# Kernel optimization log

Hardware: AMD Instinct MI355X
Metric: run time of the kernel (lower is better)

Reference implementation:

```python
import jax, jax.numpy as jnp
import numpy as np

B, T, C = 2, 2048, 1024
H = 16
HS = C // H  # head_size = 64


def setup_inputs() -> dict:
    key = jax.random.key(0)
    k1, k2, k3 = jax.random.split(key, 3)
    x = jax.random.normal(k1, (B, T, C), dtype=jnp.float32)
    # nn.Linear(n_embd, 3*n_embd): weight [3C, C], bias [3C]
    W = jax.random.normal(k2, (3 * C, C), dtype=jnp.float32) * (C ** -0.5)
    b = jax.random.normal(k3, (3 * C,), dtype=jnp.float32) * 0.02
    return {"x": x, "W": W, "b": b}


def reference(x, W, b):
    Bs, Ts, Cs = x.shape
    # fused QKV projection: [B,T,3C]
    qkv = x @ W.T + b
    qkv = qkv.reshape(Bs, Ts, 3, H, HS)
    q, k, v = jnp.moveaxis(qkv, 2, 0)          # each [B,T,H,HS]
    q = q.transpose(0, 2, 1, 3)                 # [B,H,T,HS]
    k = k.transpose(0, 2, 1, 3)
    v = v.transpose(0, 2, 1, 3)
    scale = HS ** -0.5
    wei = jnp.einsum('bhqd,bhkd->bhqk', q, k) * scale  # [B,H,T,T]
    causal = jnp.tril(jnp.ones((Ts, Ts), dtype=bool))
    wei = jnp.where(causal, wei, -jnp.inf)
    wei = jax.nn.softmax(wei, axis=-1)
    out = jnp.einsum('bhqk,bhkd->bhqd', wei, v)        # [B,H,T,HS]
    return out.transpose(0, 2, 1, 3).reshape(Bs, Ts, Cs)
```

## Files before the change

kernel.cpp:

```cpp
#include <hip/hip_runtime.h>
#include <hip/hip_bf16.h>

typedef __attribute__((ext_vector_type(8))) short bf16x8;
typedef __attribute__((ext_vector_type(4))) float f32x4;

#define BATCH 2
#define T_SEQ 2048
#define C_EMB 1024
#define NH 16
#define HS 64

__device__ __forceinline__ void gld_lds16(const __hip_bfloat16* g, __hip_bfloat16* l) {
    __builtin_amdgcn_global_load_lds((const __attribute__((address_space(1))) uint32_t*)g,
                                     (__attribute__((address_space(3))) uint32_t*)l, 16, 0, 0);
}

__global__ void cvt_f32_bf16(const float4* __restrict__ s0, ushort4* __restrict__ d0, int n40,
                             const float4* __restrict__ s1, ushort4* __restrict__ d1, int n41) {
    int i = blockIdx.x * blockDim.x + threadIdx.x;
    const float4* s; ushort4* d; int j;
    if (i < n40)            { s = s0; d = d0; j = i; }
    else if (i < n40 + n41) { s = s1; d = d1; j = i - n40; }
    else return;
    float4 v = s[j];
    ushort4 o;
    __hip_bfloat16 h;
    h = __float2bfloat16(v.x); o.x = *(ushort*)&h;
    h = __float2bfloat16(v.y); o.y = *(ushort*)&h;
    h = __float2bfloat16(v.z); o.z = *(ushort*)&h;
    h = __float2bfloat16(v.w); o.w = *(ushort*)&h;
    d[j] = o;
}

#define NT_K 16

__launch_bounds__(512, 2)
__global__ void qkv_gemm(const __hip_bfloat16* __restrict__ xb,
                         const __hip_bfloat16* __restrict__ wb,
                         const float* __restrict__ bias,
                         __hip_bfloat16* __restrict__ qo,
                         __hip_bfloat16* __restrict__ ko,
                         __hip_bfloat16* __restrict__ vto)
{
    __shared__ __align__(16) char smem[131072];
    __hip_bfloat16* ASB = (__hip_bfloat16*)smem;
    __hip_bfloat16* BSB = (__hip_bfloat16*)(smem + 65536);
    const int K = C_EMB;
    const int nTn = (3 * C_EMB) / 256;
    int bid = blockIdx.x;
    int wgid = (bid & 7) * 24 + (bid >> 3);
    int bm = wgid / nTn, bn = wgid % nTn;
    int m0 = bm * 256, n0 = bn * 256;
    int tid  = threadIdx.x;
    int lane = tid & 63, w = tid >> 6;
    int wr = w >> 2, wc = w & 3;
    int c = lane & 15, g = lane >> 4;
    int sr = lane >> 2;
    int sj = (lane & 3) ^ ((sr >> 1) & 3);
    int rchnk = (g ^ ((c >> 1) & 3)) << 4;

#define STAGE_A(kt, kh, buf) \
    { _Pragma("unroll") for (int i_ = 0; i_ < 2; ++i_) { \
        int r0_ = w * 32 + i_ * 16; \
        gld_lds16(&xb[(size_t)(m0 + r0_ + sr) * K + (kt) * 64 + (kh) * 32 + sj * 8], \
                  &ASB[((buf) * 2 + (kh)) * 8192 + r0_ * 32]); } }
#define STAGE_B(kt, kh, buf) \
    { _Pragma("unroll") for (int i_ = 0; i_ < 2; ++i_) { \
        int r0_ = w * 32 + i_ * 16; \
        gld_lds16(&wb[(size_t)(n0 + r0_ + sr) * K + (kt) * 64 + (kh) * 32 + sj * 8], \
                  &BSB[((buf) * 2 + (kh)) * 8192 + r0_ * 32]); } }

    f32x4 acc[8][4];
#pragma unroll
    for (int mi = 0; mi < 8; ++mi)
#pragma unroll
        for (int ni = 0; ni < 4; ++ni)
            acc[mi][ni] = (f32x4){0.f, 0.f, 0.f, 0.f};

    STAGE_A(0, 0, 0); STAGE_B(0, 0, 0);
    STAGE_A(0, 1, 0); STAGE_B(0, 1, 0);
    STAGE_A(1, 0, 1); STAGE_B(1, 0, 1);
    asm volatile("s_waitcnt vmcnt(4)" ::: "memory");
    __builtin_amdgcn_s_barrier();

    for (int t = 0; t < NT_K; ++t) {
        int buf = t & 1;
#pragma unroll
        for (int ks = 0; ks < 2; ++ks) {
            const __hip_bfloat16* AL = &ASB[(buf * 2 + ks) * 8192];
            const __hip_bfloat16* BL = &BSB[(buf * 2 + ks) * 8192];
            bf16x8 af[8], bfr[4];
#pragma unroll
            for (int mi = 0; mi < 8; ++mi)
                af[mi] = *(const bf16x8*)((const char*)AL + (wr * 128 + mi * 16 + c) * 64 + rchnk);
#pragma unroll
            for (int ni = 0; ni < 4; ++ni)
                bfr[ni] = *(const bf16x8*)((const char*)BL + (wc * 64 + ni * 16 + c) * 64 + rchnk);
            if (ks == 0) {
                if (t + 1 < NT_K) { STAGE_A(t + 1, 1, buf ^ 1); STAGE_B(t + 1, 1, buf ^ 1); }
            } else {
                if (t + 2 < NT_K) { STAGE_A(t + 2, 0, buf); STAGE_B(t + 2, 0, buf); }
            }
            __builtin_amdgcn_s_barrier();
            asm volatile("s_waitcnt lgkmcnt(0)" ::: "memory");
            __builtin_amdgcn_s_setprio(1);
#pragma unroll
            for (int mi = 0; mi < 8; ++mi)
#pragma unroll
                for (int ni = 0; ni < 4; ++ni)
                    acc[mi][ni] = __builtin_amdgcn_mfma_f32_16x16x32_bf16(af[mi], bfr[ni], acc[mi][ni], 0, 0, 0);
            __builtin_amdgcn_s_setprio(0);
            if (ks == 1) {
                if (t + 2 < NT_K) asm volatile("s_waitcnt vmcnt(4)" ::: "memory");
                else              asm volatile("s_waitcnt vmcnt(0)" ::: "memory");
            }
            __builtin_amdgcn_s_barrier();
        }
    }
#undef STAGE_A
#undef STAGE_B

    const float QSCALE = 0.125f * 1.44269504088896340736f;
    if (bn < 8) {
        const bool isQ = (bn < 4);
        __hip_bfloat16* dst = isQ ? qo : ko;
        float scale = isQ ? QSCALE : 1.0f;
        int h = (bn * 4 + wc) & (NH - 1);
        int b = m0 >> 11;
        size_t bhb = (size_t)(b * NH + h) * T_SEQ;
#pragma unroll
        for (int ni = 0; ni < 4; ++ni) {
            int d = ni * 16 + c;
            float bv = bias[n0 + wc * 64 + d];
#pragma unroll
            for (int mi = 0; mi < 8; ++mi) {
#pragma unroll
                for (int r = 0; r < 4; ++r) {
                    int tt = (m0 & (T_SEQ - 1)) + wr * 128 + mi * 16 + g * 4 + r;
                    float v = (acc[mi][ni][r] + bv) * scale;
                    dst[(bhb + tt) * HS + d] = __float2bfloat16(v);
                }
            }
        }
    } else {
        __syncthreads();
        char* tb = smem + w * 16384;
        int h = (bn - 8) * 4 + wc;
#pragma unroll
        for (int ni = 0; ni < 4; ++ni) {
            int d = ni * 16 + c;
            float bv = bias[n0 + wc * 64 + d];
#pragma unroll
            for (int mi = 0; mi < 8; ++mi) {
#pragma unroll
                for (int r = 0; r < 4; ++r) {
                    int m = mi * 16 + g * 4 + r;
                    __hip_bfloat16 hv = __float2bfloat16(acc[mi][ni][r] + bv);
                    *(ushort*)(tb + d * 256 + (((m >> 3) ^ c) << 4) + (m & 7) * 2) = *(ushort*)&hv;
                }
            }
        }
        int b = m0 >> 11;
        int t0 = (m0 & (T_SEQ - 1)) + wr * 128;
        size_t bh = (size_t)(b * NH + h);
        int c2 = lane & 15, g2 = lane >> 4;
#pragma unroll
        for (int it = 0; it < 16; ++it) {
            int d = it * 4 + g2;
            bf16x8 vv = *(bf16x8*)(tb + d * 256 + ((c2 ^ (d & 15)) << 4));
            *(bf16x8*)(&vto[(bh * HS + d) * T_SEQ + t0 + c2 * 8]) = vv;
        }
    }
}

#define PLDT 72

__launch_bounds__(256, 2)
__global__ void attn_fwd(const __hip_bfloat16* __restrict__ qb,
                         const __hip_bfloat16* __restrict__ kb,
                         const __hip_bfloat16* __restrict__ vtb,
                         float* __restrict__ out)
{
    __shared__ __align__(16) __hip_bfloat16 k_lds[3][64 * 64];
    __shared__ __align__(16) __hip_bfloat16 v_lds[3][64 * 64];
    __shared__ __align__(16) __hip_bfloat16 p_lds_all[4][16 * PLDT];

    int bh = blockIdx.x & 31;
    int pp = blockIdx.x >> 5;
    int w  = threadIdx.x >> 6;
    int lane = threadIdx.x & 63;
    int c = lane & 15, g = lane >> 4;
    __hip_bfloat16* p_lds = p_lds_all[w];

    const __hip_bfloat16* Qp = qb  + (size_t)bh * T_SEQ * HS;
    const __hip_bfloat16* Kp = kb  + (size_t)bh * T_SEQ * HS;
    const __hip_bfloat16* Vp = vtb + (size_t)bh * HS * T_SEQ;
    int b = bh >> 4, h = bh & (NH - 1);

    int srow = lane >> 3;
    int scol = ((lane & 7) ^ srow) << 3;
    int swz  = (c & 7) << 4;
    int krow0 = w * 16 + srow;
    int krow1 = w * 16 + 8 + srow;

    for (int phase = 0; phase < 2; ++phase) {
        int qt = phase ? pp : 31 - pp;
        int qw = qt * 64 + w * 16;
        int ntile = qt + 1;

        bf16x8 qf[2];
        qf[0] = *(const bf16x8*)(&Qp[(size_t)(qw + c) * HS + g * 8]);
        qf[1] = *(const bf16x8*)(&Qp[(size_t)(qw + c) * HS + 32 + g * 8]);

        f32x4 oacc[4];
#pragma unroll
        for (int i = 0; i < 4; ++i) oacc[i] = (f32x4){0.f, 0.f, 0.f, 0.f};
        float lrow = 0.f;

        gld_lds16(&Kp[(size_t)krow0 * HS + scol],  &k_lds[0][(w * 16) * 64]);
        gld_lds16(&Kp[(size_t)krow1 * HS + scol],  &k_lds[0][(w * 16 + 8) * 64]);
        gld_lds16(&Vp[(size_t)krow0 * T_SEQ + scol], &v_lds[0][(w * 16) * 64]);
        gld_lds16(&Vp[(size_t)krow1 * T_SEQ + scol], &v_lds[0][(w * 16 + 8) * 64]);

        int cur = 0;
        for (int tix = 0; tix < ntile; ++tix) {
            int nb = cur + 1; if (nb == 3) nb = 0;
            if (tix + 1 < ntile) {
                int k0n = (tix + 1) * 64;
                gld_lds16(&Kp[(size_t)(k0n + krow0) * HS + scol],  &k_lds[nb][(w * 16) * 64]);
                gld_lds16(&Kp[(size_t)(k0n + krow1) * HS + scol],  &k_lds[nb][(w * 16 + 8) * 64]);
                gld_lds16(&Vp[(size_t)krow0 * T_SEQ + k0n + scol], &v_lds[nb][(w * 16) * 64]);
                gld_lds16(&Vp[(size_t)krow1 * T_SEQ + k0n + scol], &v_lds[nb][(w * 16 + 8) * 64]);
                asm volatile("s_waitcnt vmcnt(4)" ::: "memory");
            } else {
                asm volatile("s_waitcnt vmcnt(0)" ::: "memory");
            }
            __builtin_amdgcn_s_barrier();

            bool diag = (tix == ntile - 1);
            const __hip_bfloat16* KL = k_lds[cur];
            const __hip_bfloat16* VL = v_lds[cur];

            f32x4 sacc[4];
#pragma unroll
            for (int i = 0; i < 4; ++i) sacc[i] = (f32x4){0.f, 0.f, 0.f, 0.f};
            __builtin_amdgcn_s_setprio(1);
#pragma unroll
            for (int ks = 0; ks < 2; ++ks)
#pragma unroll
                for (int kc = 0; kc < 4; ++kc)
                    if (!diag || kc <= w) {
                        int rr = kc * 16 + c;
                        int colB = (ks * 64 + g * 16) ^ swz;
                        bf16x8 kf = *(const bf16x8*)(&KL[rr * 64 + (colB >> 1)]);
                        sacc[kc] = __builtin_amdgcn_mfma_f32_16x16x32_bf16(kf, qf[ks], sacc[kc], 0, 0, 0);
                    }
            __builtin_amdgcn_s_setprio(0);

#pragma unroll
            for (int kc = 0; kc < 4; ++kc) {
                float p0, p1, p2, p3;
                if (!diag) {
                    p0 = __builtin_amdgcn_exp2f(sacc[kc][0]);
                    p1 = __builtin_amdgcn_exp2f(sacc[kc][1]);
                    p2 = __builtin_amdgcn_exp2f(sacc[kc][2]);
                    p3 = __builtin_amdgcn_exp2f(sacc[kc][3]);
                } else {
                    int kbase = kc * 16 + g * 4;
                    int lim = w * 16 + c;
                    p0 = (kc <= w && kbase + 0 <= lim) ? __builtin_amdgcn_exp2f(sacc[kc][0]) : 0.f;
                    p1 = (kc <= w && kbase + 1 <= lim) ? __builtin_amdgcn_exp2f(sacc[kc][1]) : 0.f;
                    p2 = (kc <= w && kbase + 2 <= lim) ? __builtin_amdgcn_exp2f(sacc[kc][2]) : 0.f;
                    p3 = (kc <= w && kbase + 3 <= lim) ? __builtin_amdgcn_exp2f(sacc[kc][3]) : 0.f;
                }
                lrow += (p0 + p1) + (p2 + p3);
                unsigned lo = ((__builtin_bit_cast(unsigned, p0) + 0x8000u) >> 16) |
                              ((__builtin_bit_cast(unsigned, p1) + 0x8000u) & 0xffff0000u);
                unsigned hi = ((__builtin_bit_cast(unsigned, p2) + 0x8000u) >> 16) |
                              ((__builtin_bit_cast(unsigned, p3) + 0x8000u) & 0xffff0000u);
                *(uint2*)(&p_lds[c * PLDT + kc * 16 + g * 4]) = make_uint2(lo, hi);
            }

            int ksm = diag ? ((w >= 2) ? 2 : 1) : 2;
            __builtin_amdgcn_s_setprio(1);
#pragma unroll
            for (int ks = 0; ks < 2; ++ks) {
                if (ks >= ksm) break;
                bf16x8 pf = *(bf16x8*)(&p_lds[c * PLDT + ks * 32 + g * 8]);
#pragma unroll
                for (int d16 = 0; d16 < 4; ++d16) {
                    int dr = d16 * 16 + c;
                    int colB = (ks * 64 + g * 16) ^ swz;
                    bf16x8 vf = *(const bf16x8*)(&VL[dr * 64 + (colB >> 1)]);
                    oacc[d16] = __builtin_amdgcn_mfma_f32_16x16x32_bf16(vf, pf, oacc[d16], 0, 0, 0);
                }
            }
            __builtin_amdgcn_s_setprio(0);
            cur = nb;
        }

        float v = lrow;
        v += __shfl_xor(v, 16, 64);
        v += __shfl_xor(v, 32, 64);
        float linv = 1.0f / v;
        float* orow = &out[((size_t)(b * T_SEQ + qw + c)) * C_EMB + h * HS + g * 4];
#pragma unroll
        for (int d16 = 0; d16 < 4; ++d16) {
            float4 st;
            st.x = oacc[d16][0] * linv;
            st.y = oacc[d16][1] * linv;
            st.z = oacc[d16][2] * linv;
            st.w = oacc[d16][3] * linv;
            *(float4*)(&orow[d16 * 16]) = st;
        }
        __builtin_amdgcn_s_barrier();
    }
}

extern "C" void kernel_launch(void* const* d_in, const int* in_sizes, int n_in,
                              void* d_out, int out_size, void* d_ws, size_t ws_size,
                              hipStream_t stream) {
    const float* x    = (const float*)d_in[0];
    const float* W    = (const float*)d_in[1];
    const float* bias = (const float*)d_in[2];
    float* out = (float*)d_out;

    char* ws = (char*)d_ws;
    __hip_bfloat16* xb  = (__hip_bfloat16*)(ws);
    __hip_bfloat16* wb  = (__hip_bfloat16*)(ws + (8u  << 20));
    __hip_bfloat16* qo  = (__hip_bfloat16*)(ws + (14u << 20));
    __hip_bfloat16* ko  = (__hip_bfloat16*)(ws + (22u << 20));
    __hip_bfloat16* vto = (__hip_bfloat16*)(ws + (30u << 20));

    int n4x = BATCH * T_SEQ * C_EMB / 4;
    int n4w = 3 * C_EMB * C_EMB / 4;
    int n4  = n4x + n4w;
    cvt_f32_bf16<<<(n4 + 255) / 256, 256, 0, stream>>>(
        (const float4*)x, (ushort4*)xb, n4x,
        (const float4*)W, (ushort4*)wb, n4w);

    int gemm_grid = (BATCH * T_SEQ / 256) * (3 * C_EMB / 256);
    qkv_gemm<<<gemm_grid, 512, 0, stream>>>(xb, wb, bias, qo, ko, vto);

    attn_fwd<<<512, 256, 0, stream>>>(qo, ko, vto, out);
}
```

Measured before the change: 80.85 us.

## Split attention keys across waves and reduce partial outputs through LDS

The attention kernel now gives each wave a 16-key slice of every 64-key tile and all 64 query rows, instead of 16 query rows against all keys. P stays in registers and feeds a 16x16x16 MFMA directly, which removes the per-wave P round-trip through LDS. At the end, partial outputs and row sums from the four waves are exchanged and summed through shared memory. This costs 4x more Q and accumulator registers, adds an extra cross-wave reduction with barriers, and uses a smaller-K MFMA for PV that may lower MFMA efficiency.

```diff
diff --git a/kernel.cpp b/kernel.cpp
--- a/kernel.cpp
+++ b/kernel.cpp
@@ -2,6 +2,7 @@
 #include <hip/hip_bf16.h>
 
 typedef __attribute__((ext_vector_type(8))) short bf16x8;
+typedef __attribute__((ext_vector_type(4))) short short4v;
 typedef __attribute__((ext_vector_type(4))) float f32x4;
 
 #define BATCH 2
@@ -10,9 +11,19 @@
 #define NH 16
 #define HS 64
 
-__device__ __forceinline__ void gld_lds16(const __hip_bfloat16* g, __hip_bfloat16* l) {
+__device__ __forceinline__ void gld_lds16(const __hip_bfloat16* g, void* l) {
     __builtin_amdgcn_global_load_lds((const __attribute__((address_space(1))) uint32_t*)g,
                                      (__attribute__((address_space(3))) uint32_t*)l, 16, 0, 0);
+}
+
+__device__ __forceinline__ f32x4 mfma16(short4v a, short4v b, f32x4 c) {
+#if __has_builtin(__builtin_amdgcn_mfma_f32_16x16x16bf16_1k)
+    return __builtin_amdgcn_mfma_f32_16x16x16bf16_1k(a, b, c, 0, 0, 0);
+#else
+    asm volatile("v_mfma_f32_16x16x16_bf16 %0, %1, %2, %0\n\ts_nop 4"
+                 : "+v"(c) : "v"(a), "v"(b));
+    return c;
+#endif
 }
 
 __global__ void cvt_f32_bf16(const float4* __restrict__ s0, ushort4* __restrict__ d0, int n40,
@@ -173,64 +184,65 @@
     }
 }
 
-#define PLDT 72
-
 __launch_bounds__(256, 2)
 __global__ void attn_fwd(const __hip_bfloat16* __restrict__ qb,
                          const __hip_bfloat16* __restrict__ kb,
                          const __hip_bfloat16* __restrict__ vtb,
                          float* __restrict__ out)
 {
-    __shared__ __align__(16) __hip_bfloat16 k_lds[3][64 * 64];
-    __shared__ __align__(16) __hip_bfloat16 v_lds[3][64 * 64];
-    __shared__ __align__(16) __hip_bfloat16 p_lds_all[4][16 * PLDT];
+    __shared__ __align__(16) char smem[50176];
 
     int bh = blockIdx.x & 31;
     int pp = blockIdx.x >> 5;
     int w  = threadIdx.x >> 6;
     int lane = threadIdx.x & 63;
     int c = lane & 15, g = lane >> 4;
-    __hip_bfloat16* p_lds = p_lds_all[w];
 
     const __hip_bfloat16* Qp = qb  + (size_t)bh * T_SEQ * HS;
     const __hip_bfloat16* Kp = kb  + (size_t)bh * T_SEQ * HS;
     const __hip_bfloat16* Vp = vtb + (size_t)bh * HS * T_SEQ;
     int b = bh >> 4, h = bh & (NH - 1);
 
-    int srow = lane >> 3;
-    int scol = ((lane & 7) ^ srow) << 3;
-    int swz  = (c & 7) << 4;
-    int krow0 = w * 16 + srow;
-    int krow1 = w * 16 + 8 + srow;
+    int l8r = lane >> 3;
+    int kscol = ((lane & 7) ^ l8r) << 3;
+    int vrow = lane >> 1, vhalf = lane & 1;
+    int kswz = (c & 7);
+
+#define ATT_STAGE(t_, buf_) { \
+    int k0_ = (t_) * 64 + w * 16; \
+    char* kb_ = smem + (buf_) * 16384 + w * 2048; \
+    char* vb_ = smem + (buf_) * 16384 + 8192 + w * 2048; \
+    gld_lds16(&Kp[(size_t)(k0_ + l8r) * HS + kscol],        kb_); \
+    gld_lds16(&Kp[(size_t)(k0_ + 8 + l8r) * HS + kscol],    kb_ + 1024); \
+    gld_lds16(&Vp[(size_t)vrow * T_SEQ + k0_ + vhalf * 8],        vb_); \
+    gld_lds16(&Vp[(size_t)(32 + vrow) * T_SEQ + k0_ + vhalf * 8], vb_ + 1024); }
 
     for (int phase = 0; phase < 2; ++phase) {
         int qt = phase ? pp : 31 - pp;
-        int qw = qt * 64 + w * 16;
+        int qw0 = qt * 64;
         int ntile = qt + 1;
 
-        bf16x8 qf[2];
-        qf[0] = *(const bf16x8*)(&Qp[(size_t)(qw + c) * HS + g * 8]);
-        qf[1] = *(const bf16x8*)(&Qp[(size_t)(qw + c) * HS + 32 + g * 8]);
-
-        f32x4 oacc[4];
-#pragma unroll
-        for (int i = 0; i < 4; ++i) oacc[i] = (f32x4){0.f, 0.f, 0.f, 0.f};
-        float lrow = 0.f;
-
-        gld_lds16(&Kp[(size_t)krow0 * HS + scol],  &k_lds[0][(w * 16) * 64]);
-        gld_lds16(&Kp[(size_t)krow1 * HS + scol],  &k_lds[0][(w * 16 + 8) * 64]);
-        gld_lds16(&Vp[(size_t)krow0 * T_SEQ + scol], &v_lds[0][(w * 16) * 64]);
-        gld_lds16(&Vp[(size_t)krow1 * T_SEQ + scol], &v_lds[0][(w * 16 + 8) * 64]);
-
+        bf16x8 qf[2][4];
+#pragma unroll
+        for (int ks = 0; ks < 2; ++ks)
+#pragma unroll
+            for (int qg = 0; qg < 4; ++qg)
+                qf[ks][qg] = *(const bf16x8*)(&Qp[(size_t)(qw0 + qg * 16 + c) * HS + ks * 32 + g * 8]);
+
+        f32x4 oacc[4][4];
+#pragma unroll
+        for (int qg = 0; qg < 4; ++qg)
+#pragma unroll
+            for (int d16 = 0; d16 < 4; ++d16)
+                oacc[qg][d16] = (f32x4){0.f, 0.f, 0.f, 0.f};
+        float lrp[4] = {0.f, 0.f, 0.f, 0.f};
+
+        ATT_STAGE(0, 0);
         int cur = 0;
         for (int tix = 0; tix < ntile; ++tix) {
             int nb = cur + 1; if (nb == 3) nb = 0;
             if (tix + 1 < ntile) {
-                int k0n = (tix + 1) * 64;
-                gld_lds16(&Kp[(size_t)(k0n + krow0) * HS + scol],  &k_lds[nb][(w * 16) * 64]);
-                gld_lds16(&Kp[(size_t)(k0n + krow1) * HS + scol],  &k_lds[nb][(w * 16 + 8) * 64]);
-                gld_lds16(&Vp[(size_t)krow0 * T_SEQ + k0n + scol], &v_lds[nb][(w * 16) * 64]);
-                gld_lds16(&Vp[(size_t)krow1 * T_SEQ + k0n + scol], &v_lds[nb][(w * 16 + 8) * 64]);
+                ATT_STAGE(tix + 1, nb);
                 asm volatile("s_waitcnt vmcnt(4)" ::: "memory");
             } else {
                 asm volatile("s_waitcnt vmcnt(0)" ::: "memory");
@@ -238,83 +250,109 @@
             __builtin_amdgcn_s_barrier();
 
             bool diag = (tix == ntile - 1);
-            const __hip_bfloat16* KL = k_lds[cur];
-            const __hip_bfloat16* VL = v_lds[cur];
+            const char* kreg = smem + cur * 16384 + w * 2048;
+            const char* vreg = smem + cur * 16384 + 8192 + w * 2048;
+
+            bf16x8 kf0 = *(const bf16x8*)(kreg + c * 128 + ((g ^ kswz) << 4));
+            bf16x8 kf1 = *(const bf16x8*)(kreg + c * 128 + (((4 + g) ^ kswz) << 4));
 
             f32x4 sacc[4];
 #pragma unroll
-            for (int i = 0; i < 4; ++i) sacc[i] = (f32x4){0.f, 0.f, 0.f, 0.f};
+            for (int qg = 0; qg < 4; ++qg) sacc[qg] = (f32x4){0.f, 0.f, 0.f, 0.f};
             __builtin_amdgcn_s_setprio(1);
 #pragma unroll
-            for (int ks = 0; ks < 2; ++ks)
-#pragma unroll
-                for (int kc = 0; kc < 4; ++kc)
-                    if (!diag || kc <= w) {
-                        int rr = kc * 16 + c;
-                        int colB = (ks * 64 + g * 16) ^ swz;
-                        bf16x8 kf = *(const bf16x8*)(&KL[rr * 64 + (colB >> 1)]);
-                        sacc[kc] = __builtin_amdgcn_mfma_f32_16x16x32_bf16(kf, qf[ks], sacc[kc], 0, 0, 0);
+            for (int qg = 0; qg < 4; ++qg)
+                if (!diag || qg >= w) {
+                    sacc[qg] = __builtin_amdgcn_mfma_f32_16x16x32_bf16(kf0, qf[0][qg], sacc[qg], 0, 0, 0);
+                    sacc[qg] = __builtin_amdgcn_mfma_f32_16x16x32_bf16(kf1, qf[1][qg], sacc[qg], 0, 0, 0);
+                }
+            __builtin_amdgcn_s_setprio(0);
+
+            short4v pf[4];
+#pragma unroll
+            for (int qg = 0; qg < 4; ++qg) {
+                pf[qg] = (short4v){0, 0, 0, 0};
+                if (!diag || qg >= w) {
+                    float p0 = __builtin_amdgcn_exp2f(sacc[qg][0]);
+                    float p1 = __builtin_amdgcn_exp2f(sacc[qg][1]);
+                    float p2 = __builtin_amdgcn_exp2f(sacc[qg][2]);
+                    float p3 = __builtin_amdgcn_exp2f(sacc[qg][3]);
+                    if (diag && qg == w) {
+                        p0 = (g * 4 + 0 <= c) ? p0 : 0.f;
+                        p1 = (g * 4 + 1 <= c) ? p1 : 0.f;
+                        p2 = (g * 4 + 2 <= c) ? p2 : 0.f;
+                        p3 = (g * 4 + 3 <= c) ? p3 : 0.f;
                     }
-            __builtin_amdgcn_s_setprio(0);
-
-#pragma unroll
-            for (int kc = 0; kc < 4; ++kc) {
-                float p0, p1, p2, p3;
-                if (!diag) {
-                    p0 = __builtin_amdgcn_exp2f(sacc[kc][0]);
-                    p1 = __builtin_amdgcn_exp2f(sacc[kc][1]);
-                    p2 = __builtin_amdgcn_exp2f(sacc[kc][2]);
-                    p3 = __builtin_amdgcn_exp2f(sacc[kc][3]);
-                } else {
-                    int kbase = kc * 16 + g * 4;
-                    int lim = w * 16 + c;
-                    p0 = (kc <= w && kbase + 0 <= lim) ? __builtin_amdgcn_exp2f(sacc[kc][0]) : 0.f;
-                    p1 = (kc <= w && kbase + 1 <= lim) ? __builtin_amdgcn_exp2f(sacc[kc][1]) : 0.f;
-                    p2 = (kc <= w && kbase + 2 <= lim) ? __builtin_amdgcn_exp2f(sacc[kc][2]) : 0.f;
-                    p3 = (kc <= w && kbase + 3 <= lim) ? __builtin_amdgcn_exp2f(sacc[kc][3]) : 0.f;
+                    lrp[qg] += (p0 + p1) + (p2 + p3);
+                    unsigned lo = ((__builtin_bit_cast(unsigned, p0) + 0x8000u) >> 16) |
+                                  ((__builtin_bit_cast(unsigned, p1) + 0x8000u) & 0xffff0000u);
+                    unsigned hi = ((__builtin_bit_cast(unsigned, p2) + 0x8000u) >> 16) |
+                                  ((__builtin_bit_cast(unsigned, p3) + 0x8000u) & 0xffff0000u);
+                    uint2 pk = make_uint2(lo, hi);
+                    pf[qg] = __builtin_bit_cast(short4v, pk);
                 }
-                lrow += (p0 + p1) + (p2 + p3);
-                unsigned lo = ((__builtin_bit_cast(unsigned, p0) + 0x8000u) >> 16) |
-                              ((__builtin_bit_cast(unsigned, p1) + 0x8000u) & 0xffff0000u);
-                unsigned hi = ((__builtin_bit_cast(unsigned, p2) + 0x8000u) >> 16) |
-                              ((__builtin_bit_cast(unsigned, p3) + 0x8000u) & 0xffff0000u);
-                *(uint2*)(&p_lds[c * PLDT + kc * 16 + g * 4]) = make_uint2(lo, hi);
-            }
-
-            int ksm = diag ? ((w >= 2) ? 2 : 1) : 2;
+            }
+
+            short4v vf[4];
+#pragma unroll
+            for (int d16 = 0; d16 < 4; ++d16)
+                vf[d16] = *(const short4v*)(vreg + (d16 * 16 + c) * 32 + g * 8);
+
             __builtin_amdgcn_s_setprio(1);
 #pragma unroll
-            for (int ks = 0; ks < 2; ++ks) {
-                if (ks >= ksm) break;
-                bf16x8 pf = *(bf16x8*)(&p_lds[c * PLDT + ks * 32 + g * 8]);
-#pragma unroll
-                for (int d16 = 0; d16 < 4; ++d16) {
-                    int dr = d16 * 16 + c;
-                    int colB = (ks * 64 + g * 16) ^ swz;
-                    bf16x8 vf = *(const bf16x8*)(&VL[dr * 64 + (colB >> 1)]);
-                    oacc[d16] = __builtin_amdgcn_mfma_f32_16x16x32_bf16(vf, pf, oacc[d16], 0, 0, 0);
-                }
-            }
+            for (int qg = 0; qg < 4; ++qg)
+                if (!diag || qg >= w)
+#pragma unroll
+                    for (int d16 = 0; d16 < 4; ++d16)
+                        oacc[qg][d16] = mfma16(vf[d16], pf[qg], oacc[qg][d16]);
             __builtin_amdgcn_s_setprio(0);
             cur = nb;
         }
 
-        float v = lrow;
-        v += __shfl_xor(v, 16, 64);
-        v += __shfl_xor(v, 32, 64);
-        float linv = 1.0f / v;
-        float* orow = &out[((size_t)(b * T_SEQ + qw + c)) * C_EMB + h * HS + g * 4];
-#pragma unroll
-        for (int d16 = 0; d16 < 4; ++d16) {
+        __builtin_amdgcn_s_barrier();
+        float* lrbuf = (float*)(smem + 49152);
+#pragma unroll
+        for (int qg = 0; qg < 4; ++qg) {
+            float v = lrp[qg];
+            v += __shfl_xor(v, 16, 64);
+            v += __shfl_xor(v, 32, 64);
+            lrp[qg] = v;
+        }
+        if (g == 0) {
+#pragma unroll
+            for (int qg = 0; qg < 4; ++qg)
+                lrbuf[(qg * 16 + c) * 4 + w] = lrp[qg];
+        }
+#pragma unroll
+        for (int dq = 0; dq < 4; ++dq)
+            if (dq != w) {
+                int slot = (w < dq) ? w : w - 1;
+                char* base = smem + dq * 12288 + slot * 4096;
+#pragma unroll
+                for (int qg = 0; qg < 4; ++qg)
+                    *(f32x4*)(base + qg * 1024 + c * 64 + g * 16) = oacc[qg][dq];
+            }
+        __builtin_amdgcn_s_barrier();
+
+#pragma unroll
+        for (int qg = 0; qg < 4; ++qg) {
+            f32x4 own = (w == 0) ? oacc[qg][0] : (w == 1) ? oacc[qg][1]
+                      : (w == 2) ? oacc[qg][2] : oacc[qg][3];
+#pragma unroll
+            for (int slot = 0; slot < 3; ++slot) {
+                f32x4 p = *(const f32x4*)(smem + w * 12288 + slot * 4096 + qg * 1024 + c * 64 + g * 16);
+                own += p;
+            }
+            f32x4 ls = *(const f32x4*)(&lrbuf[(qg * 16 + c) * 4]);
+            float linv = 1.0f / (ls[0] + ls[1] + ls[2] + ls[3]);
             float4 st;
-            st.x = oacc[d16][0] * linv;
-            st.y = oacc[d16][1] * linv;
-            st.z = oacc[d16][2] * linv;
-            st.w = oacc[d16][3] * linv;
-            *(float4*)(&orow[d16 * 16]) = st;
+            st.x = own[0] * linv; st.y = own[1] * linv;
+            st.z = own[2] * linv; st.w = own[3] * linv;
+            *(float4*)(&out[((size_t)(b * T_SEQ + qw0 + qg * 16 + c)) * C_EMB + h * HS + w * 16 + g * 4]) = st;
         }
         __builtin_amdgcn_s_barrier();
     }
+#undef ATT_STAGE
 }
 
 extern "C" void kernel_launch(void* const* d_in, const int* in_sizes, int n_in,
```

After: 81.79 us. No clear change (+1.2%).

## Split attention into one query tile per block with double-buffered LDS

Applied to the files above, without the earlier changes.

Each attention block used to process two paired query tiles (heavy plus light) one after the other. Now every block handles a single query tile, so the grid doubles to 1024 blocks, launched heaviest-first. The K/V ring shrinks from triple to double buffering, with a full vmcnt(0) wait before each barrier. The P staging buffer switches from padded rows to an XOR-swizzled layout, which cuts LDS to 40 KB and lets launch bounds ask for 4 blocks per CU. This trades the load balance of tile pairing and prefetch depth for more occupancy and latency hiding through concurrent blocks.

```diff
diff --git a/kernel.cpp b/kernel.cpp
--- a/kernel.cpp
+++ b/kernel.cpp
@@ -10,7 +10,7 @@
 #define NH 16
 #define HS 64
 
-__device__ __forceinline__ void gld_lds16(const __hip_bfloat16* g, __hip_bfloat16* l) {
+__device__ __forceinline__ void gld_lds16(const __hip_bfloat16* g, void* l) {
     __builtin_amdgcn_global_load_lds((const __attribute__((address_space(1))) uint32_t*)g,
                                      (__attribute__((address_space(3))) uint32_t*)l, 16, 0, 0);
 }
@@ -173,24 +173,21 @@
     }
 }
 
-#define PLDT 72
-
-__launch_bounds__(256, 2)
+__launch_bounds__(256, 4)
 __global__ void attn_fwd(const __hip_bfloat16* __restrict__ qb,
                          const __hip_bfloat16* __restrict__ kb,
                          const __hip_bfloat16* __restrict__ vtb,
                          float* __restrict__ out)
 {
-    __shared__ __align__(16) __hip_bfloat16 k_lds[3][64 * 64];
-    __shared__ __align__(16) __hip_bfloat16 v_lds[3][64 * 64];
-    __shared__ __align__(16) __hip_bfloat16 p_lds_all[4][16 * PLDT];
-
-    int bh = blockIdx.x & 31;
-    int pp = blockIdx.x >> 5;
+    __shared__ __align__(16) char smem[40960];
+
+    int idx = blockIdx.x;
+    int bh = idx & 31;
+    int qt = 31 - (idx >> 5);
     int w  = threadIdx.x >> 6;
     int lane = threadIdx.x & 63;
     int c = lane & 15, g = lane >> 4;
-    __hip_bfloat16* p_lds = p_lds_all[w];
+    char* p_strip = smem + 32768 + w * 2048;
 
     const __hip_bfloat16* Qp = qb  + (size_t)bh * T_SEQ * HS;
     const __hip_bfloat16* Kp = kb  + (size_t)bh * T_SEQ * HS;
@@ -202,119 +199,113 @@
     int swz  = (c & 7) << 4;
     int krow0 = w * 16 + srow;
     int krow1 = w * 16 + 8 + srow;
-
-    for (int phase = 0; phase < 2; ++phase) {
-        int qt = phase ? pp : 31 - pp;
-        int qw = qt * 64 + w * 16;
-        int ntile = qt + 1;
-
-        bf16x8 qf[2];
-        qf[0] = *(const bf16x8*)(&Qp[(size_t)(qw + c) * HS + g * 8]);
-        qf[1] = *(const bf16x8*)(&Qp[(size_t)(qw + c) * HS + 32 + g * 8]);
-
-        f32x4 oacc[4];
-#pragma unroll
-        for (int i = 0; i < 4; ++i) oacc[i] = (f32x4){0.f, 0.f, 0.f, 0.f};
-        float lrow = 0.f;
-
-        gld_lds16(&Kp[(size_t)krow0 * HS + scol],  &k_lds[0][(w * 16) * 64]);
-        gld_lds16(&Kp[(size_t)krow1 * HS + scol],  &k_lds[0][(w * 16 + 8) * 64]);
-        gld_lds16(&Vp[(size_t)krow0 * T_SEQ + scol], &v_lds[0][(w * 16) * 64]);
-        gld_lds16(&Vp[(size_t)krow1 * T_SEQ + scol], &v_lds[0][(w * 16 + 8) * 64]);
-
-        int cur = 0;
-        for (int tix = 0; tix < ntile; ++tix) {
-            int nb = cur + 1; if (nb == 3) nb = 0;
-            if (tix + 1 < ntile) {
-                int k0n = (tix + 1) * 64;
-                gld_lds16(&Kp[(size_t)(k0n + krow0) * HS + scol],  &k_lds[nb][(w * 16) * 64]);
-                gld_lds16(&Kp[(size_t)(k0n + krow1) * HS + scol],  &k_lds[nb][(w * 16 + 8) * 64]);
-                gld_lds16(&Vp[(size_t)krow0 * T_SEQ + k0n + scol], &v_lds[nb][(w * 16) * 64]);
-                gld_lds16(&Vp[(size_t)krow1 * T_SEQ + k0n + scol], &v_lds[nb][(w * 16 + 8) * 64]);
-                asm volatile("s_waitcnt vmcnt(4)" ::: "memory");
+    int qw = qt * 64 + w * 16;
+    int ntile = qt + 1;
+
+    bf16x8 qf[2];
+    qf[0] = *(const bf16x8*)(&Qp[(size_t)(qw + c) * HS + g * 8]);
+    qf[1] = *(const bf16x8*)(&Qp[(size_t)(qw + c) * HS + 32 + g * 8]);
+
+    f32x4 oacc[4];
+#pragma unroll
+    for (int i = 0; i < 4; ++i) oacc[i] = (f32x4){0.f, 0.f, 0.f, 0.f};
+    float lrow = 0.f;
+
+#define ATT_STAGE(t_, buf_) { \
+    int k0_ = (t_) * 64; \
+    char* kb_ = smem + (buf_) * 8192; \
+    char* vb_ = smem + 16384 + (buf_) * 8192; \
+    gld_lds16(&Kp[(size_t)(k0_ + krow0) * HS + scol],  kb_ + (w * 16) * 128); \
+    gld_lds16(&Kp[(size_t)(k0_ + krow1) * HS + scol],  kb_ + (w * 16 + 8) * 128); \
+    gld_lds16(&Vp[(size_t)krow0 * T_SEQ + k0_ + scol], vb_ + (w * 16) * 128); \
+    gld_lds16(&Vp[(size_t)krow1 * T_SEQ + k0_ + scol], vb_ + (w * 16 + 8) * 128); }
+
+    ATT_STAGE(0, 0);
+
+    for (int tix = 0; tix < ntile; ++tix) {
+        int cur = tix & 1;
+        asm volatile("s_waitcnt vmcnt(0)" ::: "memory");
+        __builtin_amdgcn_s_barrier();
+        if (tix + 1 < ntile) ATT_STAGE(tix + 1, cur ^ 1);
+
+        bool diag = (tix == ntile - 1);
+        const char* KL = smem + cur * 8192;
+        const char* VL = smem + 16384 + cur * 8192;
+
+        f32x4 sacc[4];
+#pragma unroll
+        for (int i = 0; i < 4; ++i) sacc[i] = (f32x4){0.f, 0.f, 0.f, 0.f};
+        __builtin_amdgcn_s_setprio(1);
+#pragma unroll
+        for (int ks = 0; ks < 2; ++ks)
+#pragma unroll
+            for (int kc = 0; kc < 4; ++kc)
+                if (!diag || kc <= w) {
+                    int rr = kc * 16 + c;
+                    int colB = (ks * 64 + g * 16) ^ swz;
+                    bf16x8 kf = *(const bf16x8*)(KL + rr * 128 + colB);
+                    sacc[kc] = __builtin_amdgcn_mfma_f32_16x16x32_bf16(kf, qf[ks], sacc[kc], 0, 0, 0);
+                }
+        __builtin_amdgcn_s_setprio(0);
+
+#pragma unroll
+        for (int kc = 0; kc < 4; ++kc) {
+            float p0, p1, p2, p3;
+            if (!diag) {
+                p0 = __builtin_amdgcn_exp2f(sacc[kc][0]);
+                p1 = __builtin_amdgcn_exp2f(sacc[kc][1]);
+                p2 = __builtin_amdgcn_exp2f(sacc[kc][2]);
+                p3 = __builtin_amdgcn_exp2f(sacc[kc][3]);
             } else {
-                asm volatile("s_waitcnt vmcnt(0)" ::: "memory");
-            }
-            __builtin_amdgcn_s_barrier();
-
-            bool diag = (tix == ntile - 1);
-            const __hip_bfloat16* KL = k_lds[cur];
-            const __hip_bfloat16* VL = v_lds[cur];
-
-            f32x4 sacc[4];
-#pragma unroll
-            for (int i = 0; i < 4; ++i) sacc[i] = (f32x4){0.f, 0.f, 0.f, 0.f};
-            __builtin_amdgcn_s_setprio(1);
-#pragma unroll
-            for (int ks = 0; ks < 2; ++ks)
-#pragma unroll
-                for (int kc = 0; kc < 4; ++kc)
-                    if (!diag || kc <= w) {
-                        int rr = kc * 16 + c;
-                        int colB = (ks * 64 + g * 16) ^ swz;
-                        bf16x8 kf = *(const bf16x8*)(&KL[rr * 64 + (colB >> 1)]);
-                        sacc[kc] = __builtin_amdgcn_mfma_f32_16x16x32_bf16(kf, qf[ks], sacc[kc], 0, 0, 0);
-                    }
-            __builtin_amdgcn_s_setprio(0);
-
-#pragma unroll
-            for (int kc = 0; kc < 4; ++kc) {
-                float p0, p1, p2, p3;
-                if (!diag) {
-                    p0 = __builtin_amdgcn_exp2f(sacc[kc][0]);
-                    p1 = __builtin_amdgcn_exp2f(sacc[kc][1]);
-                    p2 = __builtin_amdgcn_exp2f(sacc[kc][2]);
-                    p3 = __builtin_amdgcn_exp2f(sacc[kc][3]);
-                } else {
-                    int kbase = kc * 16 + g * 4;
-                    int lim = w * 16 + c;
-                    p0 = (kc <= w && kbase + 0 <= lim) ? __builtin_amdgcn_exp2f(sacc[kc][0]) : 0.f;
-                    p1 = (kc <= w && kbase + 1 <= lim) ? __builtin_amdgcn_exp2f(sacc[kc][1]) : 0.f;
-                    p2 = (kc <= w && kbase + 2 <= lim) ? __builtin_amdgcn_exp2f(sacc[kc][2]) : 0.f;
-                    p3 = (kc <= w && kbase + 3 <= lim) ? __builtin_amdgcn_exp2f(sacc[kc][3]) : 0.f;
-                }
-                lrow += (p0 + p1) + (p2 + p3);
-                unsigned lo = ((__builtin_bit_cast(unsigned, p0) + 0x8000u) >> 16) |
-                              ((__builtin_bit_cast(unsigned, p1) + 0x8000u) & 0xffff0000u);
-                unsigned hi = ((__builtin_bit_cast(unsigned, p2) + 0x8000u) >> 16) |
-                              ((__builtin_bit_cast(unsigned, p3) + 0x8000u) & 0xffff0000u);
-                *(uint2*)(&p_lds[c * PLDT + kc * 16 + g * 4]) = make_uint2(lo, hi);
-            }
-
-            int ksm = diag ? ((w >= 2) ? 2 : 1) : 2;
-            __builtin_amdgcn_s_setprio(1);
-#pragma unroll
-            for (int ks = 0; ks < 2; ++ks) {
-                if (ks >= ksm) break;
-                bf16x8 pf = *(bf16x8*)(&p_lds[c * PLDT + ks * 32 + g * 8]);
-#pragma unroll
-                for (int d16 = 0; d16 < 4; ++d16) {
-                    int dr = d16 * 16 + c;
-                    int colB = (ks * 64 + g * 16) ^ swz;
-                    bf16x8 vf = *(const bf16x8*)(&VL[dr * 64 + (colB >> 1)]);
-                    oacc[d16] = __builtin_amdgcn_mfma_f32_16x16x32_bf16(vf, pf, oacc[d16], 0, 0, 0);
-                }
-            }
-            __builtin_amdgcn_s_setprio(0);
-            cur = nb;
-        }
-
-        float v = lrow;
-        v += __shfl_xor(v, 16, 64);
-        v += __shfl_xor(v, 32, 64);
-        float linv = 1.0f / v;
-        float* orow = &out[((size_t)(b * T_SEQ + qw + c)) * C_EMB + h * HS + g * 4];
-#pragma unroll
-        for (int d16 = 0; d16 < 4; ++d16) {
-            float4 st;
-            st.x = oacc[d16][0] * linv;
-            st.y = oacc[d16][1] * linv;
-            st.z = oacc[d16][2] * linv;
-            st.w = oacc[d16][3] * linv;
-            *(float4*)(&orow[d16 * 16]) = st;
-        }
-        __builtin_amdgcn_s_barrier();
+                int kbase = kc * 16 + g * 4;
+                int lim = w * 16 + c;
+                p0 = (kc <= w && kbase + 0 <= lim) ? __builtin_amdgcn_exp2f(sacc[kc][0]) : 0.f;
+                p1 = (kc <= w && kbase + 1 <= lim) ? __builtin_amdgcn_exp2f(sacc[kc][1]) : 0.f;
+                p2 = (kc <= w && kbase + 2 <= lim) ? __builtin_amdgcn_exp2f(sacc[kc][2]) : 0.f;
+                p3 = (kc <= w && kbase + 3 <= lim) ? __builtin_amdgcn_exp2f(sacc[kc][3]) : 0.f;
+            }
+            lrow += (p0 + p1) + (p2 + p3);
+            unsigned lo = ((__builtin_bit_cast(unsigned, p0) + 0x8000u) >> 16) |
+                          ((__builtin_bit_cast(unsigned, p1) + 0x8000u) & 0xffff0000u);
+            unsigned hi = ((__builtin_bit_cast(unsigned, p2) + 0x8000u) >> 16) |
+                          ((__builtin_bit_cast(unsigned, p3) + 0x8000u) & 0xffff0000u);
+            int gran = ((kc * 2 + (g >> 1)) ^ (c & 7)) << 4;
+            *(uint2*)(p_strip + c * 128 + gran + ((g & 1) << 3)) = make_uint2(lo, hi);
+        }
+
+        int ksm = diag ? ((w >= 2) ? 2 : 1) : 2;
+        __builtin_amdgcn_s_setprio(1);
+#pragma unroll
+        for (int ks = 0; ks < 2; ++ks) {
+            if (ks >= ksm) break;
+            int pgran = ((ks * 4 + g) ^ (c & 7)) << 4;
+            bf16x8 pf = *(bf16x8*)(p_strip + c * 128 + pgran);
+#pragma unroll
+            for (int d16 = 0; d16 < 4; ++d16) {
+                int dr = d16 * 16 + c;
+                int colB = (ks * 64 + g * 16) ^ swz;
+                bf16x8 vf = *(const bf16x8*)(VL + dr * 128 + colB);
+                oacc[d16] = __builtin_amdgcn_mfma_f32_16x16x32_bf16(vf, pf, oacc[d16], 0, 0, 0);
+            }
+        }
+        __builtin_amdgcn_s_setprio(0);
     }
+
+    float v = lrow;
+    v += __shfl_xor(v, 16, 64);
+    v += __shfl_xor(v, 32, 64);
+    float linv = 1.0f / v;
+    float* orow = &out[((size_t)(b * T_SEQ + qw + c)) * C_EMB + h * HS + g * 4];
+#pragma unroll
+    for (int d16 = 0; d16 < 4; ++d16) {
+        float4 st;
+        st.x = oacc[d16][0] * linv;
+        st.y = oacc[d16][1] * linv;
+        st.z = oacc[d16][2] * linv;
+        st.w = oacc[d16][3] * linv;
+        *(float4*)(&orow[d16 * 16]) = st;
+    }
+#undef ATT_STAGE
 }
 
 extern "C" void kernel_launch(void* const* d_in, const int* in_sizes, int n_in,
@@ -342,5 +333,5 @@
     int gemm_grid = (BATCH * T_SEQ / 256) * (3 * C_EMB / 256);
     qkv_gemm<<<gemm_grid, 512, 0, stream>>>(xb, wb, bias, qo, ko, vto);
 
-    attn_fwd<<<512, 256, 0, stream>>>(qo, ko, vto, out);
-}
+    attn_fwd<<<1024, 256, 0, stream>>>(qo, ko, vto, out);
+}
```

Result: faster. 78.99 us (-2.3%).
